# Performance work log

Hardware: AMD Instinct MI355X
Metric: run time of the kernel (lower is better)

## Reference

```python
import jax, jax.numpy as jnp
import numpy as np


def setup_inputs() -> dict:
    key = jax.random.key(0)
    k1, k2, k3 = jax.random.split(key, 3)
    B, H, D, N = 2, 16, 64, 2048
    return {
        "query": jax.random.normal(k1, (B, H, D, N), dtype=jnp.float32),
        "key": jax.random.normal(k2, (B, H, D, N), dtype=jnp.float32),
        "value": jax.random.normal(k3, (B, H, D, N), dtype=jnp.float32),
    }


def reference(query, key, value):
    # NOTE: original torch code scales by sqrt(query.size(-1)) which,
    # given the [B,H,d,N] layout, is sqrt(N) (the sequence length), not sqrt(d).
    scale = query.shape[-1] ** 0.5
    # scores[b,h,q,k] = sum_d query[b,h,d,q] * key[b,h,d,k]
    scores = jnp.einsum("bhdq,bhdk->bhqk", query, key) / scale
    attn = jax.nn.softmax(scores, axis=-1)
    # out[b,h,q,v] = sum_k attn[b,h,q,k] * value[b,h,v,k]
    return jnp.einsum("bhqk,bhvk->bhqv", attn, value)
```

## Files before the change

### kernel.cpp

```cpp
#include <hip/hip_runtime.h>
#include <hip/hip_bf16.h>


typedef __attribute__((ext_vector_type(8))) short short8;
typedef __attribute__((ext_vector_type(4))) float f32x4;

#define NN 2048
#define DD 64
#define ROWB 144

#if __has_builtin(__builtin_amdgcn_exp2f)
#define EXP2(x) __builtin_amdgcn_exp2f(x)
#else
#define EXP2(x) __expf(0.69314718056f * (x))
#endif

__device__ __forceinline__ unsigned pk2(float a, float b) {
  __hip_bfloat162 hh = __float22bfloat162_rn(make_float2(a, b));
  unsigned u; __builtin_memcpy(&u, &hh, 4); return u;
}
__device__ __forceinline__ short f2bf(float f) {
  union { float f; unsigned u; } x; x.f = f;
  unsigned r = (x.u + 0x7fffu + ((x.u >> 16) & 1u)) >> 16;
  return (short)r;
}
__device__ __forceinline__ void pl32swap(unsigned &x, unsigned &y) {
  asm("v_permlane32_swap_b32 %0, %1" : "+v"(x), "+v"(y));
}
__device__ __forceinline__ void pl16swap(unsigned &x, unsigned &y) {
  asm("v_permlane16_swap_b32 %0, %1" : "+v"(x), "+v"(y));
}

__global__ __launch_bounds__(256, 3) void attn_kernel(
    const float* __restrict__ Q, const float* __restrict__ K,
    const float* __restrict__ V, float* __restrict__ Out) {
  const int tid  = threadIdx.x;
  const int wave = tid >> 6, lane = tid & 63;
  const int quad = lane >> 4, l16 = lane & 15;

  const int bh   = blockIdx.x >> 4;
  const int qblk = blockIdx.x & 15;

  const float* Qh = Q + (size_t)bh * DD * NN;
  const float* Kh = K + (size_t)bh * DD * NN;
  const float* Vh = V + (size_t)bh * DD * NN;
  float*       Oh = Out + (size_t)bh * NN * DD;

  __shared__ __align__(16) char ldsK[2][64 * ROWB];
  __shared__ __align__(16) char ldsV[2][64 * ROWB];

  const float qscale = 0.031881407f;
  const int qb = qblk * 128 + wave * 32;
  short8 bQ[2][2];
#pragma unroll
  for (int qt = 0; qt < 2; ++qt)
#pragma unroll
    for (int hh = 0; hh < 2; ++hh)
#pragma unroll
      for (int j = 0; j < 8; ++j) {
        int d = hh * 32 + quad * 8 + j;
        bQ[qt][hh][j] = f2bf(Qh[(size_t)d * NN + qb + qt * 16 + l16] * qscale);
      }

  short8 onesB;
#pragma unroll
  for (int j = 0; j < 8; ++j) onesB[j] = (short)0x3F80;

  f32x4 accO[2][4];
  f32x4 accL[2];
#pragma unroll
  for (int qt = 0; qt < 2; ++qt) {
    accL[qt] = (f32x4){0.f, 0.f, 0.f, 0.f};
#pragma unroll
    for (int vt = 0; vt < 4; ++vt) accO[qt][vt] = (f32x4){0.f, 0.f, 0.f, 0.f};
  }

  const int ka = tid & 31, kg = tid >> 5;
  const int vv = tid >> 2, vko = (tid & 3) * 16;
  const float* kbase0 = Kh + (size_t)(2 * ka) * NN + kg * 8;
  const float* kbase1 = kbase0 + NN;
  const float* vbase  = Vh + (size_t)vv * NN + vko;

  float kA[8], kB[8], vA[16];
  auto load_kv = [&](int k0) {
    const float4* p0 = (const float4*)(kbase0 + k0);
    const float4* p1 = (const float4*)(kbase1 + k0);
    float4 a0 = p0[0], a1 = p0[1];
    float4 b0 = p1[0], b1 = p1[1];
    kA[0] = a0.x; kA[1] = a0.y; kA[2] = a0.z; kA[3] = a0.w;
    kA[4] = a1.x; kA[5] = a1.y; kA[6] = a1.z; kA[7] = a1.w;
    kB[0] = b0.x; kB[1] = b0.y; kB[2] = b0.z; kB[3] = b0.w;
    kB[4] = b1.x; kB[5] = b1.y; kB[6] = b1.z; kB[7] = b1.w;
    const float4* pv = (const float4*)(vbase + k0);
    float4 c0 = pv[0], c1 = pv[1], c2 = pv[2], c3 = pv[3];
    vA[0]  = c0.x; vA[1]  = c0.y; vA[2]  = c0.z; vA[3]  = c0.w;
    vA[4]  = c1.x; vA[5]  = c1.y; vA[6]  = c1.z; vA[7]  = c1.w;
    vA[8]  = c2.x; vA[9]  = c2.y; vA[10] = c2.z; vA[11] = c2.w;
    vA[12] = c3.x; vA[13] = c3.y; vA[14] = c3.z; vA[15] = c3.w;
  };
  auto store_kv = [&](char* bK, char* bV) {
#pragma unroll
    for (int j = 0; j < 8; ++j) {
      int k = kg * 8 + j;
      int g = (ka >> 2) ^ ((k >> 1) & 7);
      *(unsigned*)&bK[k * ROWB + g * 16 + (ka & 3) * 4] = pk2(kA[j], kB[j]);
    }
    uint4 w0 = make_uint4(pk2(vA[0], vA[1]),  pk2(vA[2], vA[3]),
                          pk2(vA[4], vA[5]),  pk2(vA[6], vA[7]));
    uint4 w1 = make_uint4(pk2(vA[8], vA[9]),  pk2(vA[10], vA[11]),
                          pk2(vA[12], vA[13]), pk2(vA[14], vA[15]));
    *(uint4*)&bV[vv * ROWB + vko * 2]      = w0;
    *(uint4*)&bV[vv * ROWB + vko * 2 + 16] = w1;
  };

  load_kv(0);
  store_kv(ldsK[0], ldsV[0]);
  __syncthreads();

  const int swr = l16 >> 1;

  for (int it = 0; it < 32; ++it) {
    const int cur = it & 1;
    load_kv(((it + 1) & 31) * 64);

    const char* cK = ldsK[cur];
    const char* cV = ldsV[cur];

#pragma unroll
    for (int ks = 0; ks < 2; ++ks) {
      unsigned u[2][2][2];
#pragma unroll
      for (int k2 = 0; k2 < 2; ++k2) {
        const int kt = ks * 2 + k2;
        const char* row = &cK[(kt * 16 + l16) * ROWB];
        short8 aK0 = *(const short8*)&row[(quad ^ swr) * 16];
        short8 aK1 = *(const short8*)&row[((4 + quad) ^ swr) * 16];
#pragma unroll
        for (int qt = 0; qt < 2; ++qt) {
          f32x4 z = (f32x4){0.f, 0.f, 0.f, 0.f};
          f32x4 sT = __builtin_amdgcn_mfma_f32_16x16x32_bf16(aK0, bQ[qt][0], z, 0, 0, 0);
          sT = __builtin_amdgcn_mfma_f32_16x16x32_bf16(aK1, bQ[qt][1], sT, 0, 0, 0);
          float p0 = EXP2(sT[0]), p1 = EXP2(sT[1]);
          float p2 = EXP2(sT[2]), p3 = EXP2(sT[3]);
          u[qt][k2][0] = pk2(p0, p1);
          u[qt][k2][1] = pk2(p2, p3);
        }
      }
      short8 aP[2];
#pragma unroll
      for (int qt = 0; qt < 2; ++qt) {
        unsigned c0 = u[qt][0][0], c2 = u[qt][1][0];
        pl32swap(c0, c2); pl16swap(c0, c2);
        unsigned c1 = u[qt][0][1], c3 = u[qt][1][1];
        pl32swap(c1, c3); pl16swap(c1, c3);
        unsigned w[4] = {c0, c1, c2, c3};
        __builtin_memcpy(&aP[qt], w, 16);
        accL[qt] = __builtin_amdgcn_mfma_f32_16x16x32_bf16(aP[qt], onesB, accL[qt], 0, 0, 0);
      }
#pragma unroll
      for (int vt = 0; vt < 4; ++vt) {
        short8 bVf = *(const short8*)&cV[(vt * 16 + l16) * ROWB + ks * 64 + quad * 16];
        accO[0][vt] = __builtin_amdgcn_mfma_f32_16x16x32_bf16(aP[0], bVf, accO[0][vt], 0, 0, 0);
        accO[1][vt] = __builtin_amdgcn_mfma_f32_16x16x32_bf16(aP[1], bVf, accO[1][vt], 0, 0, 0);
      }
    }

    store_kv(ldsK[cur ^ 1], ldsV[cur ^ 1]);
    __syncthreads();
  }

#pragma unroll
  for (int qt = 0; qt < 2; ++qt)
#pragma unroll
    for (int r = 0; r < 4; ++r) {
      const float inv = 1.0f / accL[qt][r];
      const int q = qb + qt * 16 + quad * 4 + r;
#pragma unroll
      for (int vt = 0; vt < 4; ++vt)
        Oh[(size_t)q * DD + vt * 16 + l16] = accO[qt][vt][r] * inv;
    }
}

extern "C" void kernel_launch(void* const* d_in, const int* in_sizes, int n_in,
                              void* d_out, int out_size, void* d_ws, size_t ws_size,
                              hipStream_t stream) {
  const float* Q = (const float*)d_in[0];
  const float* K = (const float*)d_in[1];
  const float* V = (const float*)d_in[2];
  float* O = (float*)d_out;
  dim3 grid(2 * 16 * (NN / 128));
  attn_kernel<<<grid, dim3(256), 0, stream>>>(Q, K, V, O);
}
```

Measured before the change: 149.2 us.

## Double KV tile to 128 keys per barrier with mid-iteration staged loads

Each loop iteration now processes 128 keys instead of 64, which halves the number of __syncthreads barriers. The next tile's global loads are split into two halves, and the first half is stored to LDS partway through the compute so loads overlap MFMA work. Shared memory per block doubles and the launch-bounds occupancy hint drops from 3 to 2 blocks per CU, so there is less latency hiding from concurrent blocks.

```diff
diff --git a/kernel.cpp b/kernel.cpp
--- a/kernel.cpp
+++ b/kernel.cpp
@@ -7,7 +7,8 @@
 
 #define NN 2048
 #define DD 64
-#define ROWB 144
+#define KROWB 144
+#define VROWB 272
 
 #if __has_builtin(__builtin_amdgcn_exp2f)
 #define EXP2(x) __builtin_amdgcn_exp2f(x)
@@ -31,7 +32,7 @@
   asm("v_permlane16_swap_b32 %0, %1" : "+v"(x), "+v"(y));
 }
 
-__global__ __launch_bounds__(256, 3) void attn_kernel(
+__global__ __launch_bounds__(256, 2) void attn_kernel(
     const float* __restrict__ Q, const float* __restrict__ K,
     const float* __restrict__ V, float* __restrict__ Out) {
   const int tid  = threadIdx.x;
@@ -46,8 +47,8 @@
   const float* Vh = V + (size_t)bh * DD * NN;
   float*       Oh = Out + (size_t)bh * NN * DD;
 
-  __shared__ __align__(16) char ldsK[2][64 * ROWB];
-  __shared__ __align__(16) char ldsV[2][64 * ROWB];
+  __shared__ __align__(16) char ldsK[2][128 * KROWB];
+  __shared__ __align__(16) char ldsV[2][64 * VROWB];
 
   const float qscale = 0.031881407f;
   const int qb = qblk * 128 + wave * 32;
@@ -98,41 +99,44 @@
     vA[8]  = c2.x; vA[9]  = c2.y; vA[10] = c2.z; vA[11] = c2.w;
     vA[12] = c3.x; vA[13] = c3.y; vA[14] = c3.z; vA[15] = c3.w;
   };
-  auto store_kv = [&](char* bK, char* bV) {
+  auto store_kv = [&](char* bK, char* bV, int sub) {
 #pragma unroll
     for (int j = 0; j < 8; ++j) {
-      int k = kg * 8 + j;
-      int g = (ka >> 2) ^ ((k >> 1) & 7);
-      *(unsigned*)&bK[k * ROWB + g * 16 + (ka & 3) * 4] = pk2(kA[j], kB[j]);
+      int rowk = sub * 64 + kg * 8 + j;
+      int g = (ka >> 2) ^ ((rowk >> 1) & 7);
+      *(unsigned*)&bK[rowk * KROWB + g * 16 + (ka & 3) * 4] = pk2(kA[j], kB[j]);
     }
     uint4 w0 = make_uint4(pk2(vA[0], vA[1]),  pk2(vA[2], vA[3]),
                           pk2(vA[4], vA[5]),  pk2(vA[6], vA[7]));
     uint4 w1 = make_uint4(pk2(vA[8], vA[9]),  pk2(vA[10], vA[11]),
                           pk2(vA[12], vA[13]), pk2(vA[14], vA[15]));
-    *(uint4*)&bV[vv * ROWB + vko * 2]      = w0;
-    *(uint4*)&bV[vv * ROWB + vko * 2 + 16] = w1;
+    *(uint4*)&bV[vv * VROWB + sub * 128 + vko * 2]      = w0;
+    *(uint4*)&bV[vv * VROWB + sub * 128 + vko * 2 + 16] = w1;
   };
 
   load_kv(0);
-  store_kv(ldsK[0], ldsV[0]);
+  store_kv(ldsK[0], ldsV[0], 0);
+  load_kv(64);
+  store_kv(ldsK[0], ldsV[0], 1);
   __syncthreads();
 
   const int swr = l16 >> 1;
 
-  for (int it = 0; it < 32; ++it) {
+  for (int it = 0; it < 16; ++it) {
     const int cur = it & 1;
-    load_kv(((it + 1) & 31) * 64);
-
+    const int base = ((it + 1) & 15) * 128;
     const char* cK = ldsK[cur];
     const char* cV = ldsV[cur];
 
-#pragma unroll
-    for (int ks = 0; ks < 2; ++ks) {
+    load_kv(base);
+
+#pragma unroll
+    for (int ks = 0; ks < 4; ++ks) {
       unsigned u[2][2][2];
 #pragma unroll
       for (int k2 = 0; k2 < 2; ++k2) {
         const int kt = ks * 2 + k2;
-        const char* row = &cK[(kt * 16 + l16) * ROWB];
+        const char* row = &cK[(kt * 16 + l16) * KROWB];
         short8 aK0 = *(const short8*)&row[(quad ^ swr) * 16];
         short8 aK1 = *(const short8*)&row[((4 + quad) ^ swr) * 16];
 #pragma unroll
@@ -159,13 +163,18 @@
       }
 #pragma unroll
       for (int vt = 0; vt < 4; ++vt) {
-        short8 bVf = *(const short8*)&cV[(vt * 16 + l16) * ROWB + ks * 64 + quad * 16];
+        short8 bVf = *(const short8*)&cV[(vt * 16 + l16) * VROWB + ks * 64 + quad * 16];
         accO[0][vt] = __builtin_amdgcn_mfma_f32_16x16x32_bf16(aP[0], bVf, accO[0][vt], 0, 0, 0);
         accO[1][vt] = __builtin_amdgcn_mfma_f32_16x16x32_bf16(aP[1], bVf, accO[1][vt], 0, 0, 0);
       }
+
+      if (ks == 1) {
+        store_kv(ldsK[cur ^ 1], ldsV[cur ^ 1], 0);
+        load_kv(base + 64);
+      }
     }
 
-    store_kv(ldsK[cur ^ 1], ldsV[cur ^ 1]);
+    store_kv(ldsK[cur ^ 1], ldsV[cur ^ 1], 1);
     __syncthreads();
   }
 
```

New measurement: 146.9 us. Within noise of the previous version (-1.5%).

## Split key dimension across two blocks and combine partial outputs

Applied to the files above, without the earlier changes.

Adds a split-K variant of the attention kernel where each block processes half of the keys and writes unnormalized partial outputs and row sums to a workspace, followed by a combine kernel that sums and normalizes. The aim is to double the number of blocks so more waves run per CU and latency is hidden better. This adds extra global memory traffic for the partials and a second kernel launch. The split path only runs when a sufficiently large workspace is provided; occupancy hint also raised to 4.

```diff
diff --git a/kernel.cpp b/kernel.cpp
--- a/kernel.cpp
+++ b/kernel.cpp
@@ -8,6 +8,7 @@
 #define NN 2048
 #define DD 64
 #define ROWB 144
+#define NBH 32
 
 #if __has_builtin(__builtin_amdgcn_exp2f)
 #define EXP2(x) __builtin_amdgcn_exp2f(x)
@@ -31,20 +32,27 @@
   asm("v_permlane16_swap_b32 %0, %1" : "+v"(x), "+v"(y));
 }
 
-__global__ __launch_bounds__(256, 3) void attn_kernel(
+template <int SPLIT>
+__global__ __launch_bounds__(256, 4) void attn_kernel(
     const float* __restrict__ Q, const float* __restrict__ K,
-    const float* __restrict__ V, float* __restrict__ Out) {
+    const float* __restrict__ V, float* __restrict__ Out,
+    float* __restrict__ Opart, float* __restrict__ Lpart) {
   const int tid  = threadIdx.x;
   const int wave = tid >> 6, lane = tid & 63;
   const int quad = lane >> 4, l16 = lane & 15;
 
-  const int bh   = blockIdx.x >> 4;
-  const int qblk = blockIdx.x & 15;
+  int bh, qblk, kh;
+  if (SPLIT) {
+    bh = blockIdx.x >> 5; qblk = (blockIdx.x >> 1) & 15; kh = blockIdx.x & 1;
+  } else {
+    bh = blockIdx.x >> 4; qblk = blockIdx.x & 15; kh = 0;
+  }
+  const int kb    = SPLIT ? kh * 1024 : 0;
+  const int ITERS = SPLIT ? 16 : 32;
 
   const float* Qh = Q + (size_t)bh * DD * NN;
   const float* Kh = K + (size_t)bh * DD * NN;
   const float* Vh = V + (size_t)bh * DD * NN;
-  float*       Oh = Out + (size_t)bh * NN * DD;
 
   __shared__ __align__(16) char ldsK[2][64 * ROWB];
   __shared__ __align__(16) char ldsV[2][64 * ROWB];
@@ -77,9 +85,9 @@
 
   const int ka = tid & 31, kg = tid >> 5;
   const int vv = tid >> 2, vko = (tid & 3) * 16;
-  const float* kbase0 = Kh + (size_t)(2 * ka) * NN + kg * 8;
+  const float* kbase0 = Kh + (size_t)(2 * ka) * NN + kb + kg * 8;
   const float* kbase1 = kbase0 + NN;
-  const float* vbase  = Vh + (size_t)vv * NN + vko;
+  const float* vbase  = Vh + (size_t)vv * NN + kb + vko;
 
   float kA[8], kB[8], vA[16];
   auto load_kv = [&](int k0) {
@@ -119,9 +127,9 @@
 
   const int swr = l16 >> 1;
 
-  for (int it = 0; it < 32; ++it) {
+  for (int it = 0; it < ITERS; ++it) {
     const int cur = it & 1;
-    load_kv(((it + 1) & 31) * 64);
+    load_kv(((it + 1) & (ITERS - 1)) * 64);
 
     const char* cK = ldsK[cur];
     const char* cV = ldsV[cur];
@@ -169,16 +177,50 @@
     __syncthreads();
   }
 
-#pragma unroll
-  for (int qt = 0; qt < 2; ++qt)
-#pragma unroll
-    for (int r = 0; r < 4; ++r) {
-      const float inv = 1.0f / accL[qt][r];
-      const int q = qb + qt * 16 + quad * 4 + r;
-#pragma unroll
-      for (int vt = 0; vt < 4; ++vt)
-        Oh[(size_t)q * DD + vt * 16 + l16] = accO[qt][vt][r] * inv;
-    }
+  if (SPLIT) {
+    float* Op = Opart + (size_t)kh * ((size_t)NBH * NN * DD) + (size_t)bh * NN * DD;
+    float* Lp = Lpart + kh * (NBH * NN) + bh * NN;
+#pragma unroll
+    for (int qt = 0; qt < 2; ++qt)
+#pragma unroll
+      for (int r = 0; r < 4; ++r) {
+        const int q = qb + qt * 16 + quad * 4 + r;
+#pragma unroll
+        for (int vt = 0; vt < 4; ++vt)
+          Op[(size_t)q * DD + vt * 16 + l16] = accO[qt][vt][r];
+        if (l16 == 0) Lp[q] = accL[qt][r];
+      }
+  } else {
+    float* Oh = Out + (size_t)bh * NN * DD;
+#pragma unroll
+    for (int qt = 0; qt < 2; ++qt)
+#pragma unroll
+      for (int r = 0; r < 4; ++r) {
+        const float inv = 1.0f / accL[qt][r];
+        const int q = qb + qt * 16 + quad * 4 + r;
+#pragma unroll
+        for (int vt = 0; vt < 4; ++vt)
+          Oh[(size_t)q * DD + vt * 16 + l16] = accO[qt][vt][r] * inv;
+      }
+  }
+}
+
+__global__ __launch_bounds__(256, 8) void combine_kernel(
+    const float* __restrict__ O0, const float* __restrict__ O1,
+    const float* __restrict__ L0, const float* __restrict__ L1,
+    float* __restrict__ Out) {
+  const size_t e  = ((size_t)blockIdx.x * 256 + threadIdx.x) * 8;
+  const size_t qi = e >> 6;
+  const float linv = 1.0f / (L0[qi] + L1[qi]);
+  float4 a0 = *(const float4*)(O0 + e), a1 = *(const float4*)(O0 + e + 4);
+  float4 b0 = *(const float4*)(O1 + e), b1 = *(const float4*)(O1 + e + 4);
+  float4 r0, r1;
+  r0.x = (a0.x + b0.x) * linv; r0.y = (a0.y + b0.y) * linv;
+  r0.z = (a0.z + b0.z) * linv; r0.w = (a0.w + b0.w) * linv;
+  r1.x = (a1.x + b1.x) * linv; r1.y = (a1.y + b1.y) * linv;
+  r1.z = (a1.z + b1.z) * linv; r1.w = (a1.w + b1.w) * linv;
+  *(float4*)(Out + e)     = r0;
+  *(float4*)(Out + e + 4) = r1;
 }
 
 extern "C" void kernel_launch(void* const* d_in, const int* in_sizes, int n_in,
@@ -188,6 +230,20 @@
   const float* K = (const float*)d_in[1];
   const float* V = (const float*)d_in[2];
   float* O = (float*)d_out;
-  dim3 grid(2 * 16 * (NN / 128));
-  attn_kernel<<<grid, dim3(256), 0, stream>>>(Q, K, V, O);
-}
+
+  const size_t BHND = (size_t)NBH * NN * DD;
+  const size_t BHN  = (size_t)NBH * NN;
+  const size_t need = (2 * BHND + 2 * BHN) * sizeof(float);
+
+  if (d_ws != nullptr && ws_size >= need) {
+    float* Opart = (float*)d_ws;
+    float* Lpart = Opart + 2 * BHND;
+    attn_kernel<1><<<dim3(NBH * 16 * 2), dim3(256), 0, stream>>>(
+        Q, K, V, O, Opart, Lpart);
+    combine_kernel<<<dim3((unsigned)(BHND / (256 * 8))), dim3(256), 0, stream>>>(
+        Opart, Opart + BHND, Lpart, Lpart + BHN, O);
+  } else {
+    attn_kernel<0><<<dim3(NBH * 16), dim3(256), 0, stream>>>(
+        Q, K, V, O, nullptr, nullptr);
+  }
+}
```

Measured after the change: 149.9 us. About the same (+0.5%).

## Software-pipeline QK/softmax of next tile with PV of current via triple-buffered LDS

Applied to the files above, without the earlier changes.

Splits each iteration into an SP stage (QK^T MFMAs plus exp2) and a PV stage. SP of tile it+1 now runs alongside PV of tile it, with three LDS buffers so the stores for the tile after next do not clash. s_setprio raises priority during the PV MFMAs to help waves interleave. In exchange it holds more registers and LDS, and occupancy is dropped from 3 to 2 blocks per CU.

```diff
diff --git a/kernel.cpp b/kernel.cpp
--- a/kernel.cpp
+++ b/kernel.cpp
@@ -31,7 +31,7 @@
   asm("v_permlane16_swap_b32 %0, %1" : "+v"(x), "+v"(y));
 }
 
-__global__ __launch_bounds__(256, 3) void attn_kernel(
+__global__ __launch_bounds__(256, 2) void attn_kernel(
     const float* __restrict__ Q, const float* __restrict__ K,
     const float* __restrict__ V, float* __restrict__ Out) {
   const int tid  = threadIdx.x;
@@ -46,8 +46,9 @@
   const float* Vh = V + (size_t)bh * DD * NN;
   float*       Oh = Out + (size_t)bh * NN * DD;
 
-  __shared__ __align__(16) char ldsK[2][64 * ROWB];
-  __shared__ __align__(16) char ldsV[2][64 * ROWB];
+  __shared__ __align__(16) char lds[3][2][64 * ROWB];
+  auto bK = [&](int c) -> char* { return &lds[c % 3][0][0]; };
+  auto bV = [&](int c) -> char* { return &lds[c % 3][1][0]; };
 
   const float qscale = 0.031881407f;
   const int qb = qblk * 128 + wave * 32;
@@ -98,37 +99,26 @@
     vA[8]  = c2.x; vA[9]  = c2.y; vA[10] = c2.z; vA[11] = c2.w;
     vA[12] = c3.x; vA[13] = c3.y; vA[14] = c3.z; vA[15] = c3.w;
   };
-  auto store_kv = [&](char* bK, char* bV) {
+  auto store_kv = [&](char* dK, char* dV) {
 #pragma unroll
     for (int j = 0; j < 8; ++j) {
       int k = kg * 8 + j;
       int g = (ka >> 2) ^ ((k >> 1) & 7);
-      *(unsigned*)&bK[k * ROWB + g * 16 + (ka & 3) * 4] = pk2(kA[j], kB[j]);
+      *(unsigned*)&dK[k * ROWB + g * 16 + (ka & 3) * 4] = pk2(kA[j], kB[j]);
     }
     uint4 w0 = make_uint4(pk2(vA[0], vA[1]),  pk2(vA[2], vA[3]),
                           pk2(vA[4], vA[5]),  pk2(vA[6], vA[7]));
     uint4 w1 = make_uint4(pk2(vA[8], vA[9]),  pk2(vA[10], vA[11]),
                           pk2(vA[12], vA[13]), pk2(vA[14], vA[15]));
-    *(uint4*)&bV[vv * ROWB + vko * 2]      = w0;
-    *(uint4*)&bV[vv * ROWB + vko * 2 + 16] = w1;
-  };
-
-  load_kv(0);
-  store_kv(ldsK[0], ldsV[0]);
-  __syncthreads();
+    *(uint4*)&dV[vv * ROWB + vko * 2]      = w0;
+    *(uint4*)&dV[vv * ROWB + vko * 2 + 16] = w1;
+  };
 
   const int swr = l16 >> 1;
 
-  for (int it = 0; it < 32; ++it) {
-    const int cur = it & 1;
-    load_kv(((it + 1) & 31) * 64);
-
-    const char* cK = ldsK[cur];
-    const char* cV = ldsV[cur];
-
-#pragma unroll
-    for (int ks = 0; ks < 2; ++ks) {
-      unsigned u[2][2][2];
+  auto SP = [&](const char* cK, unsigned (&up)[2][2][2][2]) {
+#pragma unroll
+    for (int ks = 0; ks < 2; ++ks)
 #pragma unroll
       for (int k2 = 0; k2 < 2; ++k2) {
         const int kt = ks * 2 + k2;
@@ -140,18 +130,22 @@
           f32x4 z = (f32x4){0.f, 0.f, 0.f, 0.f};
           f32x4 sT = __builtin_amdgcn_mfma_f32_16x16x32_bf16(aK0, bQ[qt][0], z, 0, 0, 0);
           sT = __builtin_amdgcn_mfma_f32_16x16x32_bf16(aK1, bQ[qt][1], sT, 0, 0, 0);
-          float p0 = EXP2(sT[0]), p1 = EXP2(sT[1]);
-          float p2 = EXP2(sT[2]), p3 = EXP2(sT[3]);
-          u[qt][k2][0] = pk2(p0, p1);
-          u[qt][k2][1] = pk2(p2, p3);
+          up[ks][qt][k2][0] = pk2(EXP2(sT[0]), EXP2(sT[1]));
+          up[ks][qt][k2][1] = pk2(EXP2(sT[2]), EXP2(sT[3]));
         }
       }
+  };
+
+  auto PV = [&](const char* cV, unsigned (&up)[2][2][2][2]) {
+    __builtin_amdgcn_s_setprio(1);
+#pragma unroll
+    for (int ks = 0; ks < 2; ++ks) {
       short8 aP[2];
 #pragma unroll
       for (int qt = 0; qt < 2; ++qt) {
-        unsigned c0 = u[qt][0][0], c2 = u[qt][1][0];
+        unsigned c0 = up[ks][qt][0][0], c2 = up[ks][qt][1][0];
         pl32swap(c0, c2); pl16swap(c0, c2);
-        unsigned c1 = u[qt][0][1], c3 = u[qt][1][1];
+        unsigned c1 = up[ks][qt][0][1], c3 = up[ks][qt][1][1];
         pl32swap(c1, c3); pl16swap(c1, c3);
         unsigned w[4] = {c0, c1, c2, c3};
         __builtin_memcpy(&aP[qt], w, 16);
@@ -164,10 +158,37 @@
         accO[1][vt] = __builtin_amdgcn_mfma_f32_16x16x32_bf16(aP[1], bVf, accO[1][vt], 0, 0, 0);
       }
     }
-
-    store_kv(ldsK[cur ^ 1], ldsV[cur ^ 1]);
+    __builtin_amdgcn_s_setprio(0);
+  };
+
+  load_kv(0);
+  store_kv(bK(0), bV(0));
+  load_kv(64);
+  __syncthreads();
+
+  unsigned up[2][2][2][2], un[2][2][2][2];
+  SP(bK(0), up);
+  store_kv(bK(1), bV(1));
+  load_kv(128);
+  __syncthreads();
+
+  for (int it = 0; it < 31; ++it) {
+    SP(bK(it + 1), un);
+    PV(bV(it), up);
+    store_kv(bK(it + 2), bV(it + 2));
+    load_kv(((it + 3) & 31) * 64);
+#pragma unroll
+    for (int a = 0; a < 2; ++a)
+#pragma unroll
+      for (int b = 0; b < 2; ++b)
+#pragma unroll
+        for (int c = 0; c < 2; ++c)
+#pragma unroll
+          for (int d = 0; d < 2; ++d) up[a][b][c][d] = un[a][b][c][d];
     __syncthreads();
   }
+
+  PV(bV(31), up);
 
 #pragma unroll
   for (int qt = 0; qt < 2; ++qt)
```

Result: faster. 144.4 us (-3.2%).
